# Kernel tuning notes

Hardware: AMD Instinct MI355X
Metric: run time of the kernel (lower is better)

## Reference

```python
import jax, jax.numpy as jnp
import numpy as np

N_NODES = 100000
N_EDGES = 1600000
D_IN, D_EMB, D_POOL = 256, 128, 64
EPS = 1e-6


def setup_inputs() -> dict:
    key = jax.random.key(0)
    ks = jax.random.split(key, 10)
    x = jax.random.normal(ks[0], (N_NODES, D_IN), dtype=jnp.float32)
    edge_src = jax.random.randint(ks[1], (N_EDGES,), 0, N_NODES, dtype=jnp.int32)
    edge_dst = jax.random.randint(ks[2], (N_EDGES,), 0, N_NODES, dtype=jnp.int32)
    edge_weight = jax.random.uniform(ks[3], (N_EDGES,), dtype=jnp.float32)
    # glorot-ish init for the three GraphConvolution weights
    w1 = jax.random.normal(ks[4], (D_IN, D_EMB), dtype=jnp.float32) / np.sqrt(D_IN)
    b1 = jnp.zeros((D_EMB,), dtype=jnp.float32)
    wp = jax.random.normal(ks[5], (D_EMB, D_POOL), dtype=jnp.float32) / np.sqrt(D_EMB)
    bp = jnp.zeros((D_POOL,), dtype=jnp.float32)
    w2 = jax.random.normal(ks[6], (D_EMB, D_POOL), dtype=jnp.float32) / np.sqrt(D_EMB)
    b2 = jnp.zeros((D_POOL,), dtype=jnp.float32)
    return {"x": x, "edge_src": edge_src, "edge_dst": edge_dst,
            "edge_weight": edge_weight, "w1": w1, "b1": b1,
            "wp": wp, "bp": bp, "w2": w2, "b2": b2}


def _gcn(h, w, b, edge_src, edge_dst, edge_weight, n_nodes):
    # GraphConvolution: support = h @ w ; out = adj @ support + b (sparse spmm)
    support = h @ w                                  # [N, d_out]
    msgs = edge_weight[:, None] * support[edge_src]  # [E, d_out] gather
    agg = jax.ops.segment_sum(msgs, edge_dst, num_segments=n_nodes)
    return agg + b


def _pairnorm_si(h):
    # PairNorm mode 'PN-SI' (scale=1): center over nodes, row-wise L2 normalize
    h = h - jnp.mean(h, axis=0, keepdims=True)
    rownorm = jnp.sqrt(EPS + jnp.sum(h * h, axis=1, keepdims=True))
    return h / rownorm


def reference(x, edge_src, edge_dst, edge_weight, w1, b1, wp, bp, w2, b2):
    n = x.shape[0]
    enc1 = _gcn(x, w1, b1, edge_src, edge_dst, edge_weight, n)
    enc1 = jax.nn.relu(_pairnorm_si(enc1))
    pool1 = _gcn(enc1, wp, bp, edge_src, edge_dst, edge_weight, n)
    pool1 = jax.nn.softmax(_pairnorm_si(pool1), axis=-1)
    enc2 = _gcn(enc1, w2, b2, edge_src, edge_dst, edge_weight, n)
    enc2 = jax.nn.relu(_pairnorm_si(enc2))
    return enc2, pool1
```

## Files before the change

kernel.cpp:

```cpp
#include <hip/hip_runtime.h>
#include <stdint.h>

#define N_NODES 100000
#define N_EDGES 1600000
#define CAP 48

typedef __attribute__((ext_vector_type(8))) short bf16x8;
typedef __attribute__((ext_vector_type(4))) float f32x4;

__device__ __forceinline__ uint32_t f2bf(float f) {
  uint32_t u = __float_as_uint(f);
  u += 0x7fffu + ((u >> 16) & 1);
  return u >> 16;
}
__device__ __forceinline__ float bf_lo(uint32_t v) { return __uint_as_float(v << 16); }
__device__ __forceinline__ float bf_hi(uint32_t v) { return __uint_as_float(v & 0xffff0000u); }
__device__ __forceinline__ uint32_t pack2(float a, float b) { return f2bf(a) | (f2bf(b) << 16); }

__global__ void k_pack(const float* __restrict__ w1, const float* __restrict__ wp,
                       const float* __restrict__ w2, uint16_t* __restrict__ wT1,
                       uint16_t* __restrict__ wTc) {
  int i = blockIdx.x * 256 + threadIdx.x;
  if (i < 128 * 256) {
    int n = i >> 8, k = i & 255;
    wT1[n * 256 + (k ^ ((n & 7) << 3))] = (uint16_t)f2bf(w1[k * 128 + n]);
  }
  int j = i - 128 * 256;
  if (j >= 0 && j < 128 * 128) {
    int n = j >> 7, k = j & 127;
    wTc[n * 128 + (k ^ ((n & 7) << 3))] =
        (uint16_t)f2bf((n < 64) ? wp[k * 64 + n] : w2[k * 64 + (n - 64)]);
  }
}

__global__ __launch_bounds__(512) void k_g1s(const float* __restrict__ A,
                                             const uint16_t* __restrict__ wTs,
                                             uint16_t* __restrict__ C, int M,
                                             const int* __restrict__ esrc,
                                             const int* __restrict__ edst,
                                             const float* __restrict__ ew,
                                             int* __restrict__ fill,
                                             int2* __restrict__ rec) {
  __shared__ uint16_t bs[128 * 256];
  {
    const float4* s = (const float4*)wTs;
    float4* d = (float4*)bs;
#pragma unroll
    for (int i = 0; i < 8; i++) d[i * 512 + threadIdx.x] = s[i * 512 + threadIdx.x];
  }
  __syncthreads();

  int wave = threadIdx.x >> 6, lane = threadIdx.x & 63;
  if (wave >= 4) {
    int S = gridDim.x * 256;
    int sid = (blockIdx.x * 4 + (wave - 4)) * 64 + lane;
    for (int e = sid; e < N_EDGES; e += S) {
      int d = edst[e];
      int pos = atomicAdd(&fill[d], 1);
      rec[(size_t)d * CAP + pos] = make_int2(esrc[e], __float_as_int(ew[e]));
    }
    return;
  }

  int m0 = (blockIdx.x * 4 + wave) * 16;
  int quad = lane >> 4, mcol = lane & 15;
  int xsw = (mcol & 7) << 3;
  int arow = m0 + mcol;
  bool av = arow < M;

  float4 abuf[16];
  const float* ap = A + (size_t)arow * 256 + quad * 8;
  if (av) {
#pragma unroll
    for (int t = 0; t < 8; t++) {
      abuf[2 * t]     = *(const float4*)(ap + t * 32);
      abuf[2 * t + 1] = *(const float4*)(ap + t * 32 + 4);
    }
  } else {
#pragma unroll
    for (int t = 0; t < 16; t++) abuf[t] = (float4){0.f, 0.f, 0.f, 0.f};
  }

  const uint16_t* bp = bs + mcol * 256;

  f32x4 acc[8];
#pragma unroll
  for (int nt = 0; nt < 8; nt++) acc[nt] = (f32x4){0.f, 0.f, 0.f, 0.f};

#pragma unroll
  for (int it = 0; it < 8; it++) {
    float4 lo = abuf[2 * it], hi = abuf[2 * it + 1];
    bf16x8 a;
    a[0] = (short)f2bf(lo.x); a[1] = (short)f2bf(lo.y);
    a[2] = (short)f2bf(lo.z); a[3] = (short)f2bf(lo.w);
    a[4] = (short)f2bf(hi.x); a[5] = (short)f2bf(hi.y);
    a[6] = (short)f2bf(hi.z); a[7] = (short)f2bf(hi.w);
#pragma unroll
    for (int nt = 0; nt < 8; nt++) {
      bf16x8 b = *(const bf16x8*)(bp + nt * 4096 + ((it * 32 + quad * 8) ^ xsw));
      acc[nt] = __builtin_amdgcn_mfma_f32_16x16x32_bf16(a, b, acc[nt], 0, 0, 0);
    }
  }
#pragma unroll
  for (int r = 0; r < 4; r++) {
    int row = m0 + quad * 4 + r;
    if (row < M) {
#pragma unroll
      for (int nt = 0; nt < 8; nt++)
        C[(size_t)row * 128 + nt * 16 + mcol] = (uint16_t)f2bf(acc[nt][r]);
    }
  }
}

__global__ __launch_bounds__(256) void k_gemm2(const uint16_t* __restrict__ A,
                                               const uint16_t* __restrict__ wTs,
                                               uint16_t* __restrict__ C,
                                               const float* __restrict__ cs, int M) {
  __shared__ uint16_t bs[128 * 128];
  __shared__ float csn[128];
  {
    const float4* s = (const float4*)wTs;
    float4* d = (float4*)bs;
#pragma unroll
    for (int i = 0; i < 8; i++) d[i * 256 + threadIdx.x] = s[i * 256 + threadIdx.x];
    if (threadIdx.x < 128) csn[threadIdx.x] = cs[threadIdx.x] * (1.0f / (float)N_NODES);
  }
  __syncthreads();

  int wave = threadIdx.x >> 6, lane = threadIdx.x & 63;
  int m0 = (blockIdx.x * 4 + wave) * 16;
  int quad = lane >> 4, mcol = lane & 15;
  int xsw = (mcol & 7) << 3;
  int arow = m0 + mcol;
  bool av = arow < M;

  bf16x8 abuf[4];
  const uint16_t* ap = A + (size_t)arow * 128 + quad * 8;
  if (av) {
#pragma unroll
    for (int t = 0; t < 4; t++) abuf[t] = *(const bf16x8*)(ap + t * 32);
  } else {
#pragma unroll
    for (int t = 0; t < 4; t++) abuf[t] = (bf16x8){};
  }

  float hf[4][8];
  float ssq = 0.f;
#pragma unroll
  for (int t = 0; t < 4; t++) {
#pragma unroll
    for (int j = 0; j < 8; j++) {
      float h = av ? (__uint_as_float(((uint32_t)(uint16_t)abuf[t][j]) << 16)
                      - csn[quad * 8 + t * 32 + j])
                   : 0.f;
      hf[t][j] = h;
      ssq += h * h;
    }
  }
  ssq += __shfl_xor(ssq, 16, 64);
  ssq += __shfl_xor(ssq, 32, 64);
  float rinv = rsqrtf(1e-6f + ssq);
  bf16x8 afr[4];
#pragma unroll
  for (int t = 0; t < 4; t++)
#pragma unroll
    for (int j = 0; j < 8; j++)
      afr[t][j] = (short)f2bf(fmaxf(hf[t][j] * rinv, 0.f));

  const uint16_t* bp = bs + mcol * 128;

  f32x4 acc[8];
#pragma unroll
  for (int nt = 0; nt < 8; nt++) acc[nt] = (f32x4){0.f, 0.f, 0.f, 0.f};

#pragma unroll
  for (int it = 0; it < 4; it++) {
#pragma unroll
    for (int nt = 0; nt < 8; nt++) {
      bf16x8 b = *(const bf16x8*)(bp + nt * 2048 + ((it * 32 + quad * 8) ^ xsw));
      acc[nt] = __builtin_amdgcn_mfma_f32_16x16x32_bf16(afr[it], b, acc[nt], 0, 0, 0);
    }
  }
#pragma unroll
  for (int r = 0; r < 4; r++) {
    int row = m0 + quad * 4 + r;
    if (row < M) {
#pragma unroll
      for (int nt = 0; nt < 8; nt++)
        C[(size_t)row * 128 + nt * 16 + mcol] = (uint16_t)f2bf(acc[nt][r]);
    }
  }
}

__global__ __launch_bounds__(256) void k_spmm(const uint16_t* __restrict__ sup,
                                              const int* __restrict__ fill,
                                              const int2* __restrict__ rec,
                                              uint16_t* __restrict__ agg) {
  int wid = blockIdx.x * 4 + (threadIdx.x >> 6);
  int r0 = wid * 2;
  if (r0 >= N_NODES) return;
  int r1 = r0 + 1;
  int lane = threadIdx.x & 63;
  int c0 = fill[r0], c1 = fill[r1];
  const int2* p0 = rec + (size_t)r0 * CAP;
  const int2* p1 = rec + (size_t)r1 * CAP;
  float a00 = 0.f, a01 = 0.f, a10 = 0.f, a11 = 0.f;
  int n = c0 > c1 ? c0 : c1;
  for (int k = 0; k < n; k += 8) {
    int2 ra[8], rb[8];
    uint32_t va[8], vb[8];
    bool q0 = k < c0, q1 = k < c1;
    if (q0) {
#pragma unroll
      for (int u = 0; u < 8; u++) ra[u] = p0[k + u];
    }
    if (q1) {
#pragma unroll
      for (int u = 0; u < 8; u++) rb[u] = p1[k + u];
    }
    float wa[8], wb[8];
#pragma unroll
    for (int u = 0; u < 8; u++) {
      bool ok = q0 && (k + u < c0);
      int sidx = ok ? ra[u].x : 0;
      wa[u] = ok ? __int_as_float(ra[u].y) : 0.f;
      va[u] = *(const uint32_t*)(sup + (size_t)sidx * 128 + lane * 2);
    }
#pragma unroll
    for (int u = 0; u < 8; u++) {
      bool ok = q1 && (k + u < c1);
      int sidx = ok ? rb[u].x : 0;
      wb[u] = ok ? __int_as_float(rb[u].y) : 0.f;
      vb[u] = *(const uint32_t*)(sup + (size_t)sidx * 128 + lane * 2);
    }
#pragma unroll
    for (int u = 0; u < 8; u++) {
      a00 += wa[u] * bf_lo(va[u]);
      a01 += wa[u] * bf_hi(va[u]);
      a10 += wb[u] * bf_lo(vb[u]);
      a11 += wb[u] * bf_hi(vb[u]);
    }
  }
  *(uint32_t*)(agg + (size_t)r0 * 128 + lane * 2) = pack2(a00, a01);
  *(uint32_t*)(agg + (size_t)r1 * 128 + lane * 2) = pack2(a10, a11);
}

__global__ __launch_bounds__(256) void k_colsum(const uint16_t* __restrict__ agg,
                                                float* __restrict__ cs) {
  __shared__ float sd[256];
  int col = threadIdx.x & 127, half = threadIdx.x >> 7;
  int r0 = blockIdx.x * 256;
  float local = 0.f;
  for (int r = r0 + half; r < r0 + 256 && r < N_NODES; r += 2)
    local += __uint_as_float(((uint32_t)agg[(size_t)r * 128 + col]) << 16);
  sd[threadIdx.x] = local;
  __syncthreads();
  if (threadIdx.x < 128) atomicAdd(&cs[col], sd[threadIdx.x] + sd[threadIdx.x + 128]);
}

__global__ __launch_bounds__(256) void k_final(const uint16_t* __restrict__ agg,
                                               const float* __restrict__ cs,
                                               float* __restrict__ out) {
  int row = blockIdx.x * 4 + (threadIdx.x >> 6);
  if (row >= N_NODES) return;
  int lane = threadIdx.x & 63;
  const float invn = 1.0f / (float)N_NODES;
  uint32_t v = *(const uint32_t*)(agg + (size_t)row * 128 + lane * 2);
  float h0 = bf_lo(v) - cs[lane * 2] * invn;
  float h1 = bf_hi(v) - cs[lane * 2 + 1] * invn;
  float ss = h0 * h0 + h1 * h1;
#pragma unroll
  for (int m = 1; m < 32; m <<= 1) ss += __shfl_xor(ss, m, 64);
  float rinv = rsqrtf(1e-6f + ss);
  float p0 = h0 * rinv, p1 = h1 * rinv;
  if (lane < 32) {
    float mx = fmaxf(p0, p1);
#pragma unroll
    for (int m = 1; m < 32; m <<= 1) mx = fmaxf(mx, __shfl_xor(mx, m, 64));
    float e0 = __expf(p0 - mx), e1 = __expf(p1 - mx);
    float sum = e0 + e1;
#pragma unroll
    for (int m = 1; m < 32; m <<= 1) sum += __shfl_xor(sum, m, 64);
    float inv = 1.0f / sum;
    float2 o = {e0 * inv, e1 * inv};
    *(float2*)(out + (size_t)N_NODES * 64 + (size_t)row * 64 + lane * 2) = o;
  } else {
    int l = lane - 32;
    float2 o = {fmaxf(p0, 0.f), fmaxf(p1, 0.f)};
    *(float2*)(out + (size_t)row * 64 + l * 2) = o;
  }
}

extern "C" void kernel_launch(void* const* d_in, const int* in_sizes, int n_in,
                              void* d_out, int out_size, void* d_ws, size_t ws_size,
                              hipStream_t stream) {
  const float* x    = (const float*)d_in[0];
  const int*   esrc = (const int*)d_in[1];
  const int*   edst = (const int*)d_in[2];
  const float* ew   = (const float*)d_in[3];
  const float* w1   = (const float*)d_in[4];
  const float* wp   = (const float*)d_in[6];
  const float* w2   = (const float*)d_in[8];
  float* out = (float*)d_out;

  char* ws = (char*)d_ws;
  size_t off = 0;
  auto alloc = [&](size_t bytes) {
    char* p = ws + off;
    off += (bytes + 255) & ~(size_t)255;
    return p;
  };
  uint16_t* support = (uint16_t*)alloc((size_t)N_NODES * 128 * 2);
  uint16_t* agg     = (uint16_t*)alloc((size_t)N_NODES * 128 * 2);
  int2*     rec     = (int2*)alloc((size_t)N_NODES * CAP * 8);
  size_t zero_start = off;
  int*      fill    = (int*)alloc((size_t)N_NODES * 4);
  float*    cs      = (float*)alloc(256 * 4);
  size_t zero_bytes = off - zero_start;
  uint16_t* wT1     = (uint16_t*)alloc(128 * 256 * 2);
  uint16_t* wTc     = (uint16_t*)alloc(128 * 128 * 2);
  (void)ws_size; (void)in_sizes; (void)n_in; (void)out_size;

  hipMemsetAsync(fill, 0, zero_bytes, stream);

  k_pack<<<192, 256, 0, stream>>>(w1, wp, w2, wT1, wTc);

  k_g1s<<<(N_NODES + 63) / 64, 512, 0, stream>>>(x, wT1, support, N_NODES,
                                                 esrc, edst, ew, fill, rec);
  k_spmm<<<(N_NODES / 8), 256, 0, stream>>>(support, fill, rec, agg);
  k_colsum<<<(N_NODES + 255) / 256, 256, 0, stream>>>(agg, cs);

  k_gemm2<<<(N_NODES + 63) / 64, 256, 0, stream>>>(agg, wTc, support, cs, N_NODES);
  k_spmm<<<(N_NODES / 8), 256, 0, stream>>>(support, fill, rec, agg);
  k_colsum<<<(N_NODES + 255) / 256, 256, 0, stream>>>(agg, cs + 128);
  k_final<<<(N_NODES + 3) / 4, 256, 0, stream>>>(agg, cs + 128, out);
}
```

Before: 515.6 us.

## Fuse column-sum reduction into SpMM kernel and process more rows per wave

The SpMM kernel now accumulates per-column sums of its fp32 results for each wave, reduces them across the block in shared memory and atomically adds them to the column-sum buffer. This removes the separate colsum kernels and their re-read of the aggregated matrix. Each wave now processes 16 rows instead of 2, so the grid is much smaller. That cuts atomic traffic but leaves fewer concurrent waves to hide gather latency, and the sum is taken before bf16 rounding.

```diff
diff --git a/kernel.cpp b/kernel.cpp
--- a/kernel.cpp
+++ b/kernel.cpp
@@ -195,67 +195,71 @@
 __global__ __launch_bounds__(256) void k_spmm(const uint16_t* __restrict__ sup,
                                               const int* __restrict__ fill,
                                               const int2* __restrict__ rec,
-                                              uint16_t* __restrict__ agg) {
-  int wid = blockIdx.x * 4 + (threadIdx.x >> 6);
-  int r0 = wid * 2;
-  if (r0 >= N_NODES) return;
-  int r1 = r0 + 1;
-  int lane = threadIdx.x & 63;
-  int c0 = fill[r0], c1 = fill[r1];
-  const int2* p0 = rec + (size_t)r0 * CAP;
-  const int2* p1 = rec + (size_t)r1 * CAP;
-  float a00 = 0.f, a01 = 0.f, a10 = 0.f, a11 = 0.f;
-  int n = c0 > c1 ? c0 : c1;
-  for (int k = 0; k < n; k += 8) {
-    int2 ra[8], rb[8];
-    uint32_t va[8], vb[8];
-    bool q0 = k < c0, q1 = k < c1;
-    if (q0) {
-#pragma unroll
-      for (int u = 0; u < 8; u++) ra[u] = p0[k + u];
-    }
-    if (q1) {
-#pragma unroll
-      for (int u = 0; u < 8; u++) rb[u] = p1[k + u];
-    }
-    float wa[8], wb[8];
-#pragma unroll
-    for (int u = 0; u < 8; u++) {
-      bool ok = q0 && (k + u < c0);
-      int sidx = ok ? ra[u].x : 0;
-      wa[u] = ok ? __int_as_float(ra[u].y) : 0.f;
-      va[u] = *(const uint32_t*)(sup + (size_t)sidx * 128 + lane * 2);
-    }
-#pragma unroll
-    for (int u = 0; u < 8; u++) {
-      bool ok = q1 && (k + u < c1);
-      int sidx = ok ? rb[u].x : 0;
-      wb[u] = ok ? __int_as_float(rb[u].y) : 0.f;
-      vb[u] = *(const uint32_t*)(sup + (size_t)sidx * 128 + lane * 2);
-    }
-#pragma unroll
-    for (int u = 0; u < 8; u++) {
-      a00 += wa[u] * bf_lo(va[u]);
-      a01 += wa[u] * bf_hi(va[u]);
-      a10 += wb[u] * bf_lo(vb[u]);
-      a11 += wb[u] * bf_hi(vb[u]);
-    }
-  }
-  *(uint32_t*)(agg + (size_t)r0 * 128 + lane * 2) = pack2(a00, a01);
-  *(uint32_t*)(agg + (size_t)r1 * 128 + lane * 2) = pack2(a10, a11);
-}
-
-__global__ __launch_bounds__(256) void k_colsum(const uint16_t* __restrict__ agg,
-                                                float* __restrict__ cs) {
-  __shared__ float sd[256];
-  int col = threadIdx.x & 127, half = threadIdx.x >> 7;
-  int r0 = blockIdx.x * 256;
-  float local = 0.f;
-  for (int r = r0 + half; r < r0 + 256 && r < N_NODES; r += 2)
-    local += __uint_as_float(((uint32_t)agg[(size_t)r * 128 + col]) << 16);
-  sd[threadIdx.x] = local;
+                                              uint16_t* __restrict__ agg,
+                                              float* __restrict__ cs) {
+  int wave = threadIdx.x >> 6, lane = threadIdx.x & 63;
+  int rbase = blockIdx.x * 64 + wave * 16;
+  float c0acc = 0.f, c1acc = 0.f;
+
+  for (int pr = 0; pr < 8; ++pr) {
+    int r0 = rbase + pr * 2;
+    if (r0 >= N_NODES) break;
+    int r1 = r0 + 1;
+    int c0 = fill[r0], c1 = fill[r1];
+    const int2* p0 = rec + (size_t)r0 * CAP;
+    const int2* p1 = rec + (size_t)r1 * CAP;
+    float a00 = 0.f, a01 = 0.f, a10 = 0.f, a11 = 0.f;
+    int n = c0 > c1 ? c0 : c1;
+    for (int k = 0; k < n; k += 8) {
+      int2 ra[8], rb[8];
+      uint32_t va[8], vb[8];
+      bool q0 = k < c0, q1 = k < c1;
+      if (q0) {
+#pragma unroll
+        for (int u = 0; u < 8; u++) ra[u] = p0[k + u];
+      }
+      if (q1) {
+#pragma unroll
+        for (int u = 0; u < 8; u++) rb[u] = p1[k + u];
+      }
+      float wa[8], wb[8];
+#pragma unroll
+      for (int u = 0; u < 8; u++) {
+        bool ok = q0 && (k + u < c0);
+        int sidx = ok ? ra[u].x : 0;
+        wa[u] = ok ? __int_as_float(ra[u].y) : 0.f;
+        va[u] = *(const uint32_t*)(sup + (size_t)sidx * 128 + lane * 2);
+      }
+#pragma unroll
+      for (int u = 0; u < 8; u++) {
+        bool ok = q1 && (k + u < c1);
+        int sidx = ok ? rb[u].x : 0;
+        wb[u] = ok ? __int_as_float(rb[u].y) : 0.f;
+        vb[u] = *(const uint32_t*)(sup + (size_t)sidx * 128 + lane * 2);
+      }
+#pragma unroll
+      for (int u = 0; u < 8; u++) {
+        a00 += wa[u] * bf_lo(va[u]);
+        a01 += wa[u] * bf_hi(va[u]);
+        a10 += wb[u] * bf_lo(vb[u]);
+        a11 += wb[u] * bf_hi(vb[u]);
+      }
+    }
+    *(uint32_t*)(agg + (size_t)r0 * 128 + lane * 2) = pack2(a00, a01);
+    *(uint32_t*)(agg + (size_t)r1 * 128 + lane * 2) = pack2(a10, a11);
+    c0acc += a00 + a10;
+    c1acc += a01 + a11;
+  }
+
+  __shared__ float sd[4][128];
+  sd[wave][lane * 2]     = c0acc;
+  sd[wave][lane * 2 + 1] = c1acc;
   __syncthreads();
-  if (threadIdx.x < 128) atomicAdd(&cs[col], sd[threadIdx.x] + sd[threadIdx.x + 128]);
+  if (threadIdx.x < 128) {
+    float s = sd[0][threadIdx.x] + sd[1][threadIdx.x] +
+              sd[2][threadIdx.x] + sd[3][threadIdx.x];
+    atomicAdd(&cs[threadIdx.x], s);
+  }
 }
 
 __global__ __launch_bounds__(256) void k_final(const uint16_t* __restrict__ agg,
@@ -327,11 +331,9 @@
 
   k_g1s<<<(N_NODES + 63) / 64, 512, 0, stream>>>(x, wT1, support, N_NODES,
                                                  esrc, edst, ew, fill, rec);
-  k_spmm<<<(N_NODES / 8), 256, 0, stream>>>(support, fill, rec, agg);
-  k_colsum<<<(N_NODES + 255) / 256, 256, 0, stream>>>(agg, cs);
+  k_spmm<<<(N_NODES + 63) / 64, 256, 0, stream>>>(support, fill, rec, agg, cs);
 
   k_gemm2<<<(N_NODES + 63) / 64, 256, 0, stream>>>(agg, wTc, support, cs, N_NODES);
-  k_spmm<<<(N_NODES / 8), 256, 0, stream>>>(support, fill, rec, agg);
-  k_colsum<<<(N_NODES + 255) / 256, 256, 0, stream>>>(agg, cs + 128);
+  k_spmm<<<(N_NODES + 63) / 64, 256, 0, stream>>>(support, fill, rec, agg, cs + 128);
   k_final<<<(N_NODES + 3) / 4, 256, 0, stream>>>(agg, cs + 128, out);
 }
```

Result: no change. 523.4 us (+1.5%).
